# Kernel optimization log

Measured on AMD Instinct MI355X. Metric: run time of the kernel, lower is better.

The kernel has to match this reference:

```python
import jax, jax.numpy as jnp
import numpy as np

N, K, D, E, H, A = 50000, 12, 64, 64, 4, 16
C = 2 * D + E  # concat feature len = 192
EPS = 1e-5


def masked_bn(x, mask, gamma, beta, axes):
    # BatchNorm (training-mode batch stats) computed only over valid (mask==1) entries,
    # matching torch BN applied to PackedSequence.data.
    cnt = jnp.sum(mask) * 1.0
    mean = jnp.sum(x * mask, axis=axes) / cnt
    var = jnp.sum(jnp.square(x - mean) * mask, axis=axes) / cnt
    return gamma * (x - mean) / jnp.sqrt(var + EPS) + beta


def setup_inputs() -> dict:
    key = jax.random.key(0)
    ks = jax.random.split(key, 16)
    node_features = jax.random.normal(ks[0], (N, D), jnp.float32)
    edge_features = jax.random.normal(ks[1], (N, K, E), jnp.float32)
    neighbor_indices = jax.random.randint(ks[2], (N, K), 0, N, jnp.int32)
    # contiguous-prefix masks (pack_padded_sequence semantics), lengths in [1, K]
    lens = jax.random.randint(ks[3], (N,), 1, K + 1)
    neighbor_masks = (jnp.arange(K)[None, :] < lens[:, None]).astype(jnp.float32)
    s = 0.05
    W_edge = jax.random.normal(ks[4], (C, E), jnp.float32) * s
    b_edge = jnp.zeros((E,), jnp.float32)
    g_edge_bn = jnp.ones((E,), jnp.float32)
    b_edge_bn = jnp.zeros((E,), jnp.float32)
    W_att1 = jax.random.normal(ks[5], (H, C, A), jnp.float32) * s
    b_att1 = jnp.zeros((H, A), jnp.float32)
    W_att2 = jax.random.normal(ks[6], (H, A), jnp.float32) * s
    b_att2 = jnp.zeros((H,), jnp.float32)
    W_val = jax.random.normal(ks[7], (H, C, A), jnp.float32) * s
    b_val = jnp.zeros((H, A), jnp.float32)
    g_att_bn = jnp.ones((H, A), jnp.float32)
    b_att_bn = jnp.zeros((H, A), jnp.float32)
    g_out_bn = jnp.ones((D,), jnp.float32)
    b_out_bn = jnp.zeros((D,), jnp.float32)
    return dict(node_features=node_features, edge_features=edge_features,
                neighbor_indices=neighbor_indices, neighbor_masks=neighbor_masks,
                W_edge=W_edge, b_edge=b_edge, g_edge_bn=g_edge_bn, b_edge_bn=b_edge_bn,
                W_att1=W_att1, b_att1=b_att1, W_att2=W_att2, b_att2=b_att2,
                W_val=W_val, b_val=b_val, g_att_bn=g_att_bn, b_att_bn=b_att_bn,
                g_out_bn=g_out_bn, b_out_bn=b_out_bn)


def reference(node_features, edge_features, neighbor_indices, neighbor_masks,
              W_edge, b_edge, g_edge_bn, b_edge_bn,
              W_att1, b_att1, W_att2, b_att2, W_val, b_val,
              g_att_bn, b_att_bn, g_out_bn, b_out_bn):
    sp = jax.nn.softplus
    # fix rows with zero neighbors: mask -> [1, 0, ..., 0]
    lens = neighbor_masks.sum(axis=1)
    fix_row = jnp.zeros((K,), neighbor_masks.dtype).at[0].set(1.0)
    mask = jnp.where((lens == 0)[:, None], fix_row[None, :], neighbor_masks)  # [N,K]
    m3 = mask[:, :, None]            # [N,K,1]
    m4 = mask[:, :, None, None]      # [N,K,1,1]

    nbr = node_features[neighbor_indices]                         # [N,K,D] gather
    self_f = jnp.broadcast_to(node_features[:, None, :], (N, K, D))
    pair = jnp.concatenate([self_f, nbr], axis=2)                 # [N,K,2D]

    c1 = jnp.concatenate([pair, edge_features], axis=2)           # [N,K,C]
    e_lin = c1 @ W_edge + b_edge                                  # [N,K,E]
    e_bn = masked_bn(e_lin, m3, g_edge_bn, b_edge_bn, axes=(0, 1))
    # padded entries contribute 0 from the packed BN output (pad_packed zero-fills)
    edge_updated = sp(edge_features + e_bn * m3)                  # [N,K,E]

    c2 = jnp.concatenate([pair, edge_updated], axis=2)            # [N,K,C]

    # attention MLP per head: Linear(C->A) + softplus + Linear(A->1)
    h1 = sp(jnp.einsum('nkc,hca->nkha', c2, W_att1) + b_att1)     # [N,K,H,A]
    logits = jnp.einsum('nkha,ha->nkh', h1, W_att2) + b_att2      # [N,K,H]
    logits = jnp.where(mask[:, :, None] > 0, logits, -jnp.inf)
    att = jax.nn.softmax(logits, axis=1)                          # [N,K,H]

    v = jnp.einsum('nkc,hca->nkha', c2, W_val) + b_val            # [N,K,H,A]
    p = att[:, :, :, None] * v                                    # [N,K,H,A]
    p_bn = masked_bn(p, m4, g_att_bn, b_att_bn, axes=(0, 1))
    head_feats = sp(p_bn) * m4                                    # zero at pads
    pooled = jnp.sum(head_feats, axis=1).reshape(N, H * A)        # [N,D]

    # output BN over nodes (H*A == D, so no after-concat linear)
    mean = pooled.mean(axis=0)
    var = jnp.mean(jnp.square(pooled - mean), axis=0)
    out = g_out_bn * (pooled - mean) / jnp.sqrt(var + EPS) + b_out_bn

    node_updated = node_features + out                            # residual
    return node_updated, edge_updated
```

## Files before the change

### kernel.cpp

```cpp
#include <hip/hip_runtime.h>
#include <math.h>

#define NN 50000
#define KK 12

typedef unsigned short u16;
typedef __attribute__((ext_vector_type(4))) float f32x4;
typedef __attribute__((ext_vector_type(8))) short short8;

__device__ inline u16 f2b(float x){
  union { float f; unsigned u; } v; v.f = x;
  unsigned r = v.u + 0x7fffu + ((v.u >> 16) & 1u);
  return (u16)(r >> 16);
}
__device__ inline float b2f(u16 b){
  union { unsigned u; float f; } v; v.u = ((unsigned)b) << 16; return v.f;
}
__device__ inline float sp_(float x){
  return fmaxf(x, 0.f) + __logf(1.f + __expf(-fabsf(x)));
}
__device__ inline f32x4 mfma16(short8 a, short8 b, f32x4 c){
  return __builtin_amdgcn_mfma_f32_16x16x32_bf16(a, b, c, 0, 0, 0);
}
__device__ inline short8 ldfrag(const u16* lds, int base, int lane, int ks){
  return *(const short8*)&lds[(base + (lane & 15))*72 + ks*32 + (lane >> 4)*8];
}
__device__ inline short8 ldwfrag(const u16* wmat, int lane, int nt, int ks){
  return *(const short8*)&wmat[(nt*16 + (lane & 15))*64 + ks*32 + (lane >> 4)*8];
}
__device__ inline void stage_tile192(const float* src, u16* ldsA, int t){
  #pragma unroll
  for (int i = 0; i < 12; ++i){
    int f4 = t + i*256;
    int m = f4 >> 4, d = (f4 & 15) * 4;
    const float4 v = *(const float4*)(src + m*64 + d);
    ushort4 b; b.x = f2b(v.x); b.y = f2b(v.y); b.z = f2b(v.z); b.w = f2b(v.w);
    *(ushort4*)&ldsA[m*72 + d] = b;
  }
}

__global__ void kw_conv(const float* We, const float* Wa, const float* Wv, u16* wb){
  int gid = blockIdx.x*256 + threadIdx.x;
  if (gid >= 9*4096) return;
  int mat = gid >> 12, rem = gid & 4095;
  int j = rem >> 6, d = rem & 63;
  int fam = mat / 3, part = mat % 3;
  int c = part*64 + d;
  float v;
  if (fam == 0) v = We[c*64 + j];
  else {
    const float* W = (fam == 1) ? Wa : Wv;
    v = W[(j >> 4)*3072 + c*16 + (j & 15)];
  }
  wb[mat*4096 + j*64 + d] = f2b(v);
}

__global__ void km_mask(const float* masks, float* maskf, float* stats){
  int t = threadIdx.x;
  int n = blockIdx.x*256 + t;
  float len = 0.f;
  if (n < NN){
    float row[KK];
    #pragma unroll
    for (int k = 0; k < KK; ++k){ row[k] = masks[n*KK + k]; len += row[k]; }
    if (len == 0.f){
      #pragma unroll
      for (int k = 0; k < KK; ++k) row[k] = (k == 0) ? 1.f : 0.f;
      len = 1.f;
    }
    #pragma unroll
    for (int k = 0; k < KK; ++k) maskf[n*KK + k] = row[k];
  }
  __shared__ float red[256];
  red[t] = len; __syncthreads();
  for (int s = 128; s > 0; s >>= 1){ if (t < s) red[t] += red[t + s]; __syncthreads(); }
  if (t == 0) atomicAdd(&stats[0], red[0]);
}

__global__ __launch_bounds__(256,4) void kp_proj(const float* node, const u16* wb,
    float* ps_e, float* ps_a, float* ps_v, u16* pn_e, u16* pn_a, u16* pn_v){
  __shared__ u16 ldsA[64*72];
  int t = threadIdx.x;
  int node0 = blockIdx.x*64;
  #pragma unroll
  for (int i = 0; i < 4; ++i){
    int f4 = t + i*256;
    int m = f4 >> 4, d = (f4 & 15)*4;
    float4 v = make_float4(0.f,0.f,0.f,0.f);
    if (node0 + m < NN) v = *(const float4*)(node + (size_t)(node0 + m)*64 + d);
    ushort4 b; b.x=f2b(v.x); b.y=f2b(v.y); b.z=f2b(v.z); b.w=f2b(v.w);
    *(ushort4*)&ldsA[m*72 + d] = b;
  }
  __syncthreads();
  int lane = t & 63, w = t >> 6;
  int m0 = w*16;
  short8 a0 = ldfrag(ldsA, m0, lane, 0);
  short8 a1 = ldfrag(ldsA, m0, lane, 1);
  float* psArr[3] = {ps_e, ps_a, ps_v};
  u16*  pnArr[3] = {pn_e, pn_a, pn_v};
  #pragma unroll
  for (int p = 0; p < 6; ++p){
    const u16* W = wb + ((p % 3)*3 + (p / 3))*4096;
    #pragma unroll
    for (int nt = 0; nt < 4; ++nt){
      short8 b0 = ldwfrag(W, lane, nt, 0);
      short8 b1 = ldwfrag(W, lane, nt, 1);
      f32x4 acc = {0.f,0.f,0.f,0.f};
      acc = mfma16(a0, b0, acc);
      acc = mfma16(a1, b1, acc);
      int col = nt*16 + (lane & 15);
      #pragma unroll
      for (int r = 0; r < 4; ++r){
        int nrow = node0 + m0 + (lane >> 4)*4 + r;
        if (nrow < NN){
          if (p < 3) psArr[p][(size_t)nrow*64 + col] = acc[r];
          else       pnArr[p-3][(size_t)nrow*64 + col] = f2b(acc[r]);
        }
      }
    }
  }
}

__global__ __launch_bounds__(256,4) void k1_estats(const float* edgef, const int* nidx,
    const float* maskf, const float* ps_e, const u16* pn_e, const float* b_edge,
    const u16* wb, float* stats){
  __shared__ u16 ldsA[192*72];
  __shared__ int rPs[192]; __shared__ int rPn[192]; __shared__ float rM[192];
  __shared__ float sred[128];
  int t = threadIdx.x;
  int node0 = blockIdx.x*16;
  int e0 = node0*KK;
  stage_tile192(edgef + (size_t)e0*64, ldsA, t);
  if (t < 192){ rPs[t] = (node0 + t/KK)*64; rPn[t] = nidx[e0 + t]*64; rM[t] = maskf[e0 + t]; }
  if (t < 128) sred[t] = 0.f;
  __syncthreads();
  int lane = t & 63, w = t >> 6;
  const u16* We_ = wb + 2*4096;
  float be4[4];
  #pragma unroll
  for (int nt = 0; nt < 4; ++nt) be4[nt] = b_edge[nt*16 + (lane & 15)];
  #pragma unroll
  for (int mi = 0; mi < 3; ++mi){
    int mt = w + mi*4;
    short8 a0 = ldfrag(ldsA, mt*16, lane, 0);
    short8 a1 = ldfrag(ldsA, mt*16, lane, 1);
    #pragma unroll
    for (int nt = 0; nt < 4; ++nt){
      short8 b0 = ldwfrag(We_, lane, nt, 0);
      short8 b1 = ldwfrag(We_, lane, nt, 1);
      f32x4 acc = {0.f,0.f,0.f,0.f};
      acc = mfma16(a0, b0, acc);
      acc = mfma16(a1, b1, acc);
      int col = nt*16 + (lane & 15);
      float s = 0.f, q = 0.f;
      #pragma unroll
      for (int r = 0; r < 4; ++r){
        int row = mt*16 + (lane >> 4)*4 + r;
        float v = acc[r] + ps_e[rPs[row] + col] + b2f(pn_e[rPn[row] + col]) + be4[nt];
        float m = rM[row];
        s += v*m; q += v*v*m;
      }
      s += __shfl_xor(s, 16); s += __shfl_xor(s, 32);
      q += __shfl_xor(q, 16); q += __shfl_xor(q, 32);
      if (lane < 16){ atomicAdd(&sred[col], s); atomicAdd(&sred[64 + col], q); }
    }
  }
  __syncthreads();
  if (t < 128) atomicAdd(&stats[64 + t], sred[t]);
}

__global__ void k_fin(const float* g, const float* b, float* stats, int sumoff, int outoff, float cntfix){
  int j = threadIdx.x;
  float cnt = (cntfix > 0.f) ? cntfix : stats[0];
  float mean = stats[sumoff + j] / cnt;
  float var = stats[sumoff + 64 + j] / cnt - mean*mean;
  var = fmaxf(var, 0.f);
  float A = g[j] / sqrtf(var + 1e-5f);
  stats[outoff + j] = A;
  stats[outoff + 64 + j] = b[j] - mean*A;
}

__global__ __launch_bounds__(256,4) void k3_main(const float* edgef, const int* nidx,
    const float* maskf, const float* ps_e, const u16* pn_e, const float* ps_a, const u16* pn_a,
    const float* ps_v, const u16* pn_v, const float* b_edge, const float* b_att1,
    const float* W_att2, const float* b_att2, const float* b_val,
    const u16* wb, float* stats, float* out_edge, float* att_out, u16* p_out){
  __shared__ u16 ldsA[192*72];
  __shared__ float ldsLA[192*4];
  __shared__ int rPs[192]; __shared__ int rPn[192]; __shared__ float rM[192];
  __shared__ float sred[128];
  int t = threadIdx.x;
  int node0 = blockIdx.x*16;
  int e0 = node0*KK;
  stage_tile192(edgef + (size_t)e0*64, ldsA, t);
  if (t < 192){ rPs[t] = (node0 + t/KK)*64; rPn[t] = nidx[e0 + t]*64; rM[t] = maskf[e0 + t]; }
  if (t < 128) sred[t] = 0.f;
  __syncthreads();
  int lane = t & 63, w = t >> 6;
  int cl = lane & 15;

  {
    const u16* W = wb + 2*4096;
    float Ae4[4], Be4[4], be4[4];
    #pragma unroll
    for (int nt = 0; nt < 4; ++nt){
      int col = nt*16 + cl;
      Ae4[nt] = stats[192 + col]; Be4[nt] = stats[256 + col]; be4[nt] = b_edge[col];
    }
    #pragma unroll
    for (int mi = 0; mi < 3; ++mi){
      int mt = w + mi*4;
      short8 a0 = ldfrag(ldsA, mt*16, lane, 0);
      short8 a1 = ldfrag(ldsA, mt*16, lane, 1);
      #pragma unroll
      for (int nt = 0; nt < 4; ++nt){
        short8 b0 = ldwfrag(W, lane, nt, 0);
        short8 b1 = ldwfrag(W, lane, nt, 1);
        f32x4 acc = {0.f,0.f,0.f,0.f};
        acc = mfma16(a0, b0, acc);
        acc = mfma16(a1, b1, acc);
        int col = nt*16 + cl;
        #pragma unroll
        for (int r = 0; r < 4; ++r){
          int row = mt*16 + (lane >> 4)*4 + r;
          float elin = acc[r] + ps_e[rPs[row] + col] + b2f(pn_e[rPn[row] + col]) + be4[nt];
          float ebn = Ae4[nt]*elin + Be4[nt];
          float orig = b2f(ldsA[row*72 + col]);
          float eu = sp_(orig + ebn*rM[row]);
          out_edge[((size_t)e0 + row)*64 + col] = eu;
          ldsA[row*72 + col] = f2b(eu);
        }
      }
    }
  }
  __syncthreads();
  {
    const u16* W = wb + 5*4096;
    float w24[4], ba4[4];
    #pragma unroll
    for (int nt = 0; nt < 4; ++nt){
      int col = nt*16 + cl;
      w24[nt] = W_att2[col]; ba4[nt] = b_att1[col];
    }
    #pragma unroll
    for (int mi = 0; mi < 3; ++mi){
      int mt = w + mi*4;
      short8 a0 = ldfrag(ldsA, mt*16, lane, 0);
      short8 a1 = ldfrag(ldsA, mt*16, lane, 1);
      #pragma unroll
      for (int nt = 0; nt < 4; ++nt){
        short8 b0 = ldwfrag(W, lane, nt, 0);
        short8 b1 = ldwfrag(W, lane, nt, 1);
        f32x4 acc = {0.f,0.f,0.f,0.f};
        acc = mfma16(a0, b0, acc);
        acc = mfma16(a1, b1, acc);
        int col = nt*16 + cl;
        #pragma unroll
        for (int r = 0; r < 4; ++r){
          int row = mt*16 + (lane >> 4)*4 + r;
          float h1 = sp_(acc[r] + ps_a[rPs[row] + col] + b2f(pn_a[rPn[row] + col]) + ba4[nt]);
          float lg = h1 * w24[nt];
          lg += __shfl_xor(lg, 1); lg += __shfl_xor(lg, 2);
          lg += __shfl_xor(lg, 4); lg += __shfl_xor(lg, 8);
          if (cl == 0) ldsLA[row*4 + nt] = lg + b_att2[nt];
        }
      }
    }
  }
  __syncthreads();
  if (t < 64){
    int nl = t >> 2, h = t & 3;
    float lrow[KK], mrow[KK];
    #pragma unroll
    for (int k = 0; k < KK; ++k){ lrow[k] = ldsLA[(nl*KK + k)*4 + h]; mrow[k] = rM[nl*KK + k]; }
    float mx = -3.0e38f;
    #pragma unroll
    for (int k = 0; k < KK; ++k) if (mrow[k] > 0.f) mx = fmaxf(mx, lrow[k]);
    float ssum = 0.f; float ee[KK];
    #pragma unroll
    for (int k = 0; k < KK; ++k){ float e = (mrow[k] > 0.f) ? __expf(lrow[k] - mx) : 0.f; ee[k] = e; ssum += e; }
    float inv = 1.f / ssum;
    #pragma unroll
    for (int k = 0; k < KK; ++k){
      float a = ee[k]*inv;
      ldsLA[(nl*KK + k)*4 + h] = a;
      att_out[((size_t)(node0 + nl)*KK + k)*4 + h] = a;
    }
  }
  __syncthreads();
  {
    const u16* W = wb + 8*4096;
    float bv4[4];
    #pragma unroll
    for (int nt = 0; nt < 4; ++nt) bv4[nt] = b_val[nt*16 + cl];
    #pragma unroll
    for (int mi = 0; mi < 3; ++mi){
      int mt = w + mi*4;
      short8 a0 = ldfrag(ldsA, mt*16, lane, 0);
      short8 a1 = ldfrag(ldsA, mt*16, lane, 1);
      #pragma unroll
      for (int nt = 0; nt < 4; ++nt){
        short8 b0 = ldwfrag(W, lane, nt, 0);
        short8 b1 = ldwfrag(W, lane, nt, 1);
        f32x4 acc = {0.f,0.f,0.f,0.f};
        acc = mfma16(a0, b0, acc);
        acc = mfma16(a1, b1, acc);
        int col = nt*16 + cl;
        float s = 0.f, q = 0.f;
        #pragma unroll
        for (int r = 0; r < 4; ++r){
          int row = mt*16 + (lane >> 4)*4 + r;
          float v = acc[r] + ps_v[rPs[row] + col] + b2f(pn_v[rPn[row] + col]) + bv4[nt];
          float p = ldsLA[row*4 + nt] * v;
          float m = rM[row];
          s += p*m; q += p*p*m;
          if (p_out) p_out[((size_t)e0 + row)*64 + col] = f2b(p);
        }
        s += __shfl_xor(s, 16); s += __shfl_xor(s, 32);
        q += __shfl_xor(q, 16); q += __shfl_xor(q, 32);
        if (lane < 16){ atomicAdd(&sred[col], s); atomicAdd(&sred[64 + col], q); }
      }
    }
  }
  __syncthreads();
  if (t < 128) atomicAdd(&stats[320 + t], sred[t]);
}

__global__ void k5_stream(const u16* pbuf, const float* maskf, float* stats, float* pooled){
  __shared__ float sred[128];
  int t = threadIdx.x;
  int node0 = blockIdx.x*16;
  int col = t & 63;
  if (t < 128) sred[t] = 0.f;
  __syncthreads();
  float Ap = stats[448 + col], Bp = stats[512 + col];
  float s = 0.f, q = 0.f;
  #pragma unroll
  for (int i = 0; i < 4; ++i){
    int n = node0 + (t >> 6) + i*4;
    float acc = 0.f;
    #pragma unroll
    for (int k = 0; k < KK; ++k){
      float m = maskf[n*KK + k];
      float p = b2f(pbuf[((size_t)(n*KK + k))*64 + col]);
      acc += sp_(Ap*p + Bp) * m;
    }
    pooled[(size_t)n*64 + col] = acc;
    s += acc; q += acc*acc;
  }
  atomicAdd(&sred[col], s); atomicAdd(&sred[64 + col], q);
  __syncthreads();
  if (t < 128) atomicAdd(&stats[576 + t], sred[t]);
}

__global__ __launch_bounds__(256,4) void k5_rec(const float* eu, const int* nidx,
    const float* maskf, const float* ps_v, const u16* pn_v, const float* b_val,
    const u16* wb, const float* att_in, float* stats, float* pooled){
  __shared__ u16 ldsA[192*72];
  __shared__ float ldsAtt[192*4];
  __shared__ float pool[16*64];
  __shared__ int rPs[192]; __shared__ int rPn[192]; __shared__ float rM[192];
  __shared__ float sred[128];
  int t = threadIdx.x;
  int node0 = blockIdx.x*16;
  int e0 = node0*KK;
  stage_tile192(eu + (size_t)e0*64, ldsA, t);
  if (t < 192){ rPs[t] = (node0 + t/KK)*64; rPn[t] = nidx[e0 + t]*64; rM[t] = maskf[e0 + t]; }
  #pragma unroll
  for (int i = 0; i < 3; ++i){ int q = t + i*256; ldsAtt[q] = att_in[(size_t)e0*4 + q]; }
  #pragma unroll
  for (int i = 0; i < 4; ++i) pool[t + i*256] = 0.f;
  if (t < 128) sred[t] = 0.f;
  __syncthreads();
  int lane = t & 63, w = t >> 6;
  int cl = lane & 15;
  const u16* W = wb + 8*4096;
  float bv4[4], Ap4[4], Bp4[4];
  #pragma unroll
  for (int nt = 0; nt < 4; ++nt){
    int col = nt*16 + cl;
    bv4[nt] = b_val[col]; Ap4[nt] = stats[448 + col]; Bp4[nt] = stats[512 + col];
  }
  #pragma unroll
  for (int mi = 0; mi < 3; ++mi){
    int mt = w + mi*4;
    short8 a0 = ldfrag(ldsA, mt*16, lane, 0);
    short8 a1 = ldfrag(ldsA, mt*16, lane, 1);
    #pragma unroll
    for (int nt = 0; nt < 4; ++nt){
      short8 b0 = ldwfrag(W, lane, nt, 0);
      short8 b1 = ldwfrag(W, lane, nt, 1);
      f32x4 acc = {0.f,0.f,0.f,0.f};
      acc = mfma16(a0, b0, acc);
      acc = mfma16(a1, b1, acc);
      int col = nt*16 + cl;
      #pragma unroll
      for (int r = 0; r < 4; ++r){
        int row = mt*16 + (lane >> 4)*4 + r;
        float v = acc[r] + ps_v[rPs[row] + col] + b2f(pn_v[rPn[row] + col]) + bv4[nt];
        float p = ldsAtt[row*4 + nt] * v;
        float head = sp_(Ap4[nt]*p + Bp4[nt]) * rM[row];
        atomicAdd(&pool[(row/KK)*64 + col], head);
      }
    }
  }
  __syncthreads();
  int ch = t & 63;
  float s = 0.f, q = 0.f;
  #pragma unroll
  for (int i = 0; i < 4; ++i){
    int qi = t + i*256;
    float val = pool[qi];
    pooled[((size_t)(node0 + (qi >> 6)))*64 + ch] = val;
    s += val; q += val*val;
  }
  atomicAdd(&sred[ch], s); atomicAdd(&sred[64 + ch], q);
  __syncthreads();
  if (t < 128) atomicAdd(&stats[576 + t], sred[t]);
}

__global__ void k7_out(const float* node, const float* stats, float* out){
  int i = blockIdx.x*256 + threadIdx.x;
  if (i < NN*64){
    int ch = i & 63;
    float pooled = out[i];
    out[i] = node[i] + stats[704 + ch]*pooled + stats[768 + ch];
  }
}

extern "C" void kernel_launch(void* const* d_in, const int* in_sizes, int n_in,
                              void* d_out, int out_size, void* d_ws, size_t ws_size,
                              hipStream_t stream){
  const float* node   = (const float*)d_in[0];
  const float* edgef  = (const float*)d_in[1];
  const int*   nidx   = (const int*)d_in[2];
  const float* masks  = (const float*)d_in[3];
  const float* We     = (const float*)d_in[4];
  const float* b_edge = (const float*)d_in[5];
  const float* g_ebn  = (const float*)d_in[6];
  const float* b_ebn  = (const float*)d_in[7];
  const float* Wa1    = (const float*)d_in[8];
  const float* b_att1 = (const float*)d_in[9];
  const float* Wa2    = (const float*)d_in[10];
  const float* b_att2 = (const float*)d_in[11];
  const float* Wv     = (const float*)d_in[12];
  const float* b_val  = (const float*)d_in[13];
  const float* g_abn  = (const float*)d_in[14];
  const float* b_abn  = (const float*)d_in[15];
  const float* g_obn  = (const float*)d_in[16];
  const float* b_obn  = (const float*)d_in[17];

  float* ps_e   = (float*)d_ws;
  float* ps_a   = ps_e   + (size_t)NN*64;
  float* ps_v   = ps_a   + (size_t)NN*64;
  float* maskf  = ps_v   + (size_t)NN*64;
  float* att    = maskf  + (size_t)NN*KK;
  float* stats  = att    + (size_t)NN*KK*4;
  u16*   pn_e   = (u16*)(stats + 1024);
  u16*   pn_a   = pn_e   + (size_t)NN*64;
  u16*   pn_v   = pn_a   + (size_t)NN*64;
  u16*   wb     = pn_v   + (size_t)NN*64;
  u16*   pbuf   = wb     + 9*4096;
  size_t need   = (size_t)((char*)(pbuf + (size_t)NN*KK*64) - (char*)d_ws);
  bool   use_p  = (ws_size >= need);

  float* out_node = (float*)d_out;
  float* out_edge = out_node + (size_t)NN*64;

  hipMemsetAsync(stats, 0, 1024*sizeof(float), stream);
  kw_conv<<<144, 256, 0, stream>>>(We, Wa1, Wv, wb);
  km_mask<<<(NN + 255)/256, 256, 0, stream>>>(masks, maskf, stats);
  kp_proj<<<(NN + 63)/64, 256, 0, stream>>>(node, wb, ps_e, ps_a, ps_v, pn_e, pn_a, pn_v);
  k1_estats<<<NN/16, 256, 0, stream>>>(edgef, nidx, maskf, ps_e, pn_e, b_edge, wb, stats);
  k_fin<<<1, 64, 0, stream>>>(g_ebn, b_ebn, stats, 64, 192, 0.f);
  k3_main<<<NN/16, 256, 0, stream>>>(edgef, nidx, maskf, ps_e, pn_e, ps_a, pn_a, ps_v, pn_v,
      b_edge, b_att1, Wa2, b_att2, b_val, wb, stats, out_edge, att, use_p ? pbuf : (u16*)nullptr);
  k_fin<<<1, 64, 0, stream>>>(g_abn, b_abn, stats, 320, 448, 0.f);
  if (use_p)
    k5_stream<<<NN/16, 256, 0, stream>>>(pbuf, maskf, stats, out_node);
  else
    k5_rec<<<NN/16, 256, 0, stream>>>(out_edge, nidx, maskf, ps_v, pn_v, b_val, wb, att, stats, out_node);
  k_fin<<<1, 64, 0, stream>>>(g_obn, b_obn, stats, 576, 704, (float)NN);
  k7_out<<<(NN*64 + 255)/256, 256, 0, stream>>>(node, stats, out_node);
}
```

Baseline: 826.9 us.

## Fuse attention and value GEMMs in k3, shrink LDS metadata, vectorize k5_stream

In k3_main the attention-logit and value projections now run in a single pass over the A fragments. The value results are kept in registers as packed bf16 until the softmax finishes, which removes one reload of the LDS tiles and one phase of weight fragment reads. Per-row LDS arrays are slimmed by computing the self-node row with a multiply-shift instead of storing rPs, and by storing the mask as a byte; launch bounds rise to 5 blocks per SM. The attention output write is skipped when the streaming path is used. k5_stream now processes 4 channels per thread with vector loads and stores. The trade-off is higher register pressure from holding the value results, and a small precision loss from rounding v to bf16 before the multiply by attention.

```diff
diff --git a/kernel.cpp b/kernel.cpp
--- a/kernel.cpp
+++ b/kernel.cpp
@@ -5,6 +5,7 @@
 #define KK 12
 
 typedef unsigned short u16;
+typedef unsigned char u8;
 typedef __attribute__((ext_vector_type(4))) float f32x4;
 typedef __attribute__((ext_vector_type(8))) short short8;
 
@@ -22,6 +23,7 @@
 __device__ inline f32x4 mfma16(short8 a, short8 b, f32x4 c){
   return __builtin_amdgcn_mfma_f32_16x16x32_bf16(a, b, c, 0, 0, 0);
 }
+__device__ inline int nl_(int row){ return (row*171) >> 11; }
 __device__ inline short8 ldfrag(const u16* lds, int base, int lane, int ks){
   return *(const short8*)&lds[(base + (lane & 15))*72 + ks*32 + (lane >> 4)*8];
 }
@@ -121,24 +123,26 @@
   }
 }
 
-__global__ __launch_bounds__(256,4) void k1_estats(const float* edgef, const int* nidx,
+__global__ __launch_bounds__(256,5) void k1_estats(const float* edgef, const int* nidx,
     const float* maskf, const float* ps_e, const u16* pn_e, const float* b_edge,
     const u16* wb, float* stats){
   __shared__ u16 ldsA[192*72];
-  __shared__ int rPs[192]; __shared__ int rPn[192]; __shared__ float rM[192];
+  __shared__ int rPn[192]; __shared__ u8 m8[192];
   __shared__ float sred[128];
   int t = threadIdx.x;
   int node0 = blockIdx.x*16;
   int e0 = node0*KK;
+  int psb = node0*64;
   stage_tile192(edgef + (size_t)e0*64, ldsA, t);
-  if (t < 192){ rPs[t] = (node0 + t/KK)*64; rPn[t] = nidx[e0 + t]*64; rM[t] = maskf[e0 + t]; }
+  if (t < 192){ rPn[t] = nidx[e0 + t]*64; m8[t] = (u8)maskf[e0 + t]; }
   if (t < 128) sred[t] = 0.f;
   __syncthreads();
   int lane = t & 63, w = t >> 6;
+  int cl = lane & 15;
   const u16* We_ = wb + 2*4096;
   float be4[4];
   #pragma unroll
-  for (int nt = 0; nt < 4; ++nt) be4[nt] = b_edge[nt*16 + (lane & 15)];
+  for (int nt = 0; nt < 4; ++nt) be4[nt] = b_edge[nt*16 + cl];
   #pragma unroll
   for (int mi = 0; mi < 3; ++mi){
     int mt = w + mi*4;
@@ -151,13 +155,13 @@
       f32x4 acc = {0.f,0.f,0.f,0.f};
       acc = mfma16(a0, b0, acc);
       acc = mfma16(a1, b1, acc);
-      int col = nt*16 + (lane & 15);
+      int col = nt*16 + cl;
       float s = 0.f, q = 0.f;
       #pragma unroll
       for (int r = 0; r < 4; ++r){
         int row = mt*16 + (lane >> 4)*4 + r;
-        float v = acc[r] + ps_e[rPs[row] + col] + b2f(pn_e[rPn[row] + col]) + be4[nt];
-        float m = rM[row];
+        float v = acc[r] + ps_e[psb + nl_(row)*64 + col] + b2f(pn_e[rPn[row] + col]) + be4[nt];
+        float m = (float)m8[row];
         s += v*m; q += v*v*m;
       }
       s += __shfl_xor(s, 16); s += __shfl_xor(s, 32);
@@ -180,20 +184,21 @@
   stats[outoff + 64 + j] = b[j] - mean*A;
 }
 
-__global__ __launch_bounds__(256,4) void k3_main(const float* edgef, const int* nidx,
+__global__ __launch_bounds__(256,5) void k3_main(const float* edgef, const int* nidx,
     const float* maskf, const float* ps_e, const u16* pn_e, const float* ps_a, const u16* pn_a,
     const float* ps_v, const u16* pn_v, const float* b_edge, const float* b_att1,
     const float* W_att2, const float* b_att2, const float* b_val,
     const u16* wb, float* stats, float* out_edge, float* att_out, u16* p_out){
   __shared__ u16 ldsA[192*72];
   __shared__ float ldsLA[192*4];
-  __shared__ int rPs[192]; __shared__ int rPn[192]; __shared__ float rM[192];
+  __shared__ int rPn[192]; __shared__ u8 m8[192];
   __shared__ float sred[128];
   int t = threadIdx.x;
   int node0 = blockIdx.x*16;
   int e0 = node0*KK;
+  int psb = node0*64;
   stage_tile192(edgef + (size_t)e0*64, ldsA, t);
-  if (t < 192){ rPs[t] = (node0 + t/KK)*64; rPn[t] = nidx[e0 + t]*64; rM[t] = maskf[e0 + t]; }
+  if (t < 192){ rPn[t] = nidx[e0 + t]*64; m8[t] = (u8)maskf[e0 + t]; }
   if (t < 128) sred[t] = 0.f;
   __syncthreads();
   int lane = t & 63, w = t >> 6;
@@ -223,10 +228,10 @@
         #pragma unroll
         for (int r = 0; r < 4; ++r){
           int row = mt*16 + (lane >> 4)*4 + r;
-          float elin = acc[r] + ps_e[rPs[row] + col] + b2f(pn_e[rPn[row] + col]) + be4[nt];
+          float elin = acc[r] + ps_e[psb + nl_(row)*64 + col] + b2f(pn_e[rPn[row] + col]) + be4[nt];
           float ebn = Ae4[nt]*elin + Be4[nt];
           float orig = b2f(ldsA[row*72 + col]);
-          float eu = sp_(orig + ebn*rM[row]);
+          float eu = sp_(orig + ebn*(float)m8[row]);
           out_edge[((size_t)e0 + row)*64 + col] = eu;
           ldsA[row*72 + col] = f2b(eu);
         }
@@ -234,13 +239,15 @@
     }
   }
   __syncthreads();
+  unsigned vpk[3][4][2];
   {
-    const u16* W = wb + 5*4096;
-    float w24[4], ba4[4];
+    const u16* Wa = wb + 5*4096;
+    const u16* Wv = wb + 8*4096;
+    float w24[4], ba4[4], bv4[4];
     #pragma unroll
     for (int nt = 0; nt < 4; ++nt){
       int col = nt*16 + cl;
-      w24[nt] = W_att2[col]; ba4[nt] = b_att1[col];
+      w24[nt] = W_att2[col]; ba4[nt] = b_att1[col]; bv4[nt] = b_val[col];
     }
     #pragma unroll
     for (int mi = 0; mi < 3; ++mi){
@@ -249,8 +256,8 @@
       short8 a1 = ldfrag(ldsA, mt*16, lane, 1);
       #pragma unroll
       for (int nt = 0; nt < 4; ++nt){
-        short8 b0 = ldwfrag(W, lane, nt, 0);
-        short8 b1 = ldwfrag(W, lane, nt, 1);
+        short8 b0 = ldwfrag(Wa, lane, nt, 0);
+        short8 b1 = ldwfrag(Wa, lane, nt, 1);
         f32x4 acc = {0.f,0.f,0.f,0.f};
         acc = mfma16(a0, b0, acc);
         acc = mfma16(a1, b1, acc);
@@ -258,97 +265,113 @@
         #pragma unroll
         for (int r = 0; r < 4; ++r){
           int row = mt*16 + (lane >> 4)*4 + r;
-          float h1 = sp_(acc[r] + ps_a[rPs[row] + col] + b2f(pn_a[rPn[row] + col]) + ba4[nt]);
+          float h1 = sp_(acc[r] + ps_a[psb + nl_(row)*64 + col] + b2f(pn_a[rPn[row] + col]) + ba4[nt]);
           float lg = h1 * w24[nt];
           lg += __shfl_xor(lg, 1); lg += __shfl_xor(lg, 2);
           lg += __shfl_xor(lg, 4); lg += __shfl_xor(lg, 8);
           if (cl == 0) ldsLA[row*4 + nt] = lg + b_att2[nt];
         }
       }
-    }
-  }
-  __syncthreads();
-  if (t < 64){
-    int nl = t >> 2, h = t & 3;
-    float lrow[KK], mrow[KK];
-    #pragma unroll
-    for (int k = 0; k < KK; ++k){ lrow[k] = ldsLA[(nl*KK + k)*4 + h]; mrow[k] = rM[nl*KK + k]; }
-    float mx = -3.0e38f;
-    #pragma unroll
-    for (int k = 0; k < KK; ++k) if (mrow[k] > 0.f) mx = fmaxf(mx, lrow[k]);
-    float ssum = 0.f; float ee[KK];
-    #pragma unroll
-    for (int k = 0; k < KK; ++k){ float e = (mrow[k] > 0.f) ? __expf(lrow[k] - mx) : 0.f; ee[k] = e; ssum += e; }
-    float inv = 1.f / ssum;
-    #pragma unroll
-    for (int k = 0; k < KK; ++k){
-      float a = ee[k]*inv;
-      ldsLA[(nl*KK + k)*4 + h] = a;
-      att_out[((size_t)(node0 + nl)*KK + k)*4 + h] = a;
-    }
-  }
-  __syncthreads();
-  {
-    const u16* W = wb + 8*4096;
-    float bv4[4];
-    #pragma unroll
-    for (int nt = 0; nt < 4; ++nt) bv4[nt] = b_val[nt*16 + cl];
-    #pragma unroll
-    for (int mi = 0; mi < 3; ++mi){
-      int mt = w + mi*4;
-      short8 a0 = ldfrag(ldsA, mt*16, lane, 0);
-      short8 a1 = ldfrag(ldsA, mt*16, lane, 1);
       #pragma unroll
       for (int nt = 0; nt < 4; ++nt){
-        short8 b0 = ldwfrag(W, lane, nt, 0);
-        short8 b1 = ldwfrag(W, lane, nt, 1);
+        short8 b0 = ldwfrag(Wv, lane, nt, 0);
+        short8 b1 = ldwfrag(Wv, lane, nt, 1);
         f32x4 acc = {0.f,0.f,0.f,0.f};
         acc = mfma16(a0, b0, acc);
         acc = mfma16(a1, b1, acc);
         int col = nt*16 + cl;
-        float s = 0.f, q = 0.f;
         #pragma unroll
         for (int r = 0; r < 4; ++r){
           int row = mt*16 + (lane >> 4)*4 + r;
-          float v = acc[r] + ps_v[rPs[row] + col] + b2f(pn_v[rPn[row] + col]) + bv4[nt];
+          float v = acc[r] + ps_v[psb + nl_(row)*64 + col] + b2f(pn_v[rPn[row] + col]) + bv4[nt];
+          unsigned vb = (unsigned)f2b(v);
+          if ((r & 1) == 0) vpk[mi][nt][r >> 1] = vb;
+          else              vpk[mi][nt][r >> 1] |= (vb << 16);
+        }
+      }
+    }
+  }
+  __syncthreads();
+  if (t < 64){
+    int nl = t >> 2, h = t & 3;
+    float lrow[KK], mrow[KK];
+    #pragma unroll
+    for (int k = 0; k < KK; ++k){ lrow[k] = ldsLA[(nl*KK + k)*4 + h]; mrow[k] = (float)m8[nl*KK + k]; }
+    float mx = -3.0e38f;
+    #pragma unroll
+    for (int k = 0; k < KK; ++k) if (mrow[k] > 0.f) mx = fmaxf(mx, lrow[k]);
+    float ssum = 0.f; float ee[KK];
+    #pragma unroll
+    for (int k = 0; k < KK; ++k){ float e = (mrow[k] > 0.f) ? __expf(lrow[k] - mx) : 0.f; ee[k] = e; ssum += e; }
+    float inv = 1.f / ssum;
+    #pragma unroll
+    for (int k = 0; k < KK; ++k){
+      float a = ee[k]*inv;
+      ldsLA[(nl*KK + k)*4 + h] = a;
+      if (att_out) att_out[((size_t)(node0 + nl)*KK + k)*4 + h] = a;
+    }
+  }
+  __syncthreads();
+  {
+    float s[4] = {0.f,0.f,0.f,0.f}, q[4] = {0.f,0.f,0.f,0.f};
+    #pragma unroll
+    for (int mi = 0; mi < 3; ++mi){
+      int mt = w + mi*4;
+      #pragma unroll
+      for (int nt = 0; nt < 4; ++nt){
+        int col = nt*16 + cl;
+        #pragma unroll
+        for (int r = 0; r < 4; ++r){
+          int row = mt*16 + (lane >> 4)*4 + r;
+          unsigned pk = vpk[mi][nt][r >> 1];
+          float v = b2f((u16)((r & 1) ? (pk >> 16) : (pk & 0xffff)));
           float p = ldsLA[row*4 + nt] * v;
-          float m = rM[row];
-          s += p*m; q += p*p*m;
+          float m = (float)m8[row];
+          s[nt] += p*m; q[nt] += p*p*m;
           if (p_out) p_out[((size_t)e0 + row)*64 + col] = f2b(p);
         }
-        s += __shfl_xor(s, 16); s += __shfl_xor(s, 32);
-        q += __shfl_xor(q, 16); q += __shfl_xor(q, 32);
-        if (lane < 16){ atomicAdd(&sred[col], s); atomicAdd(&sred[64 + col], q); }
-      }
+      }
+    }
+    #pragma unroll
+    for (int nt = 0; nt < 4; ++nt){
+      float ss = s[nt], qq = q[nt];
+      ss += __shfl_xor(ss, 16); ss += __shfl_xor(ss, 32);
+      qq += __shfl_xor(qq, 16); qq += __shfl_xor(qq, 32);
+      if (lane < 16){ atomicAdd(&sred[nt*16 + cl], ss); atomicAdd(&sred[64 + nt*16 + cl], qq); }
     }
   }
   __syncthreads();
   if (t < 128) atomicAdd(&stats[320 + t], sred[t]);
 }
 
-__global__ void k5_stream(const u16* pbuf, const float* maskf, float* stats, float* pooled){
+__global__ __launch_bounds__(256,8) void k5_stream(const u16* pbuf, const float* maskf,
+    float* stats, float* pooled){
   __shared__ float sred[128];
   int t = threadIdx.x;
   int node0 = blockIdx.x*16;
-  int col = t & 63;
+  int n = node0 + (t >> 4);
+  int cg = (t & 15)*4;
   if (t < 128) sred[t] = 0.f;
   __syncthreads();
-  float Ap = stats[448 + col], Bp = stats[512 + col];
-  float s = 0.f, q = 0.f;
-  #pragma unroll
-  for (int i = 0; i < 4; ++i){
-    int n = node0 + (t >> 6) + i*4;
-    float acc = 0.f;
-    #pragma unroll
-    for (int k = 0; k < KK; ++k){
-      float m = maskf[n*KK + k];
-      float p = b2f(pbuf[((size_t)(n*KK + k))*64 + col]);
-      acc += sp_(Ap*p + Bp) * m;
-    }
-    pooled[(size_t)n*64 + col] = acc;
-    s += acc; q += acc*acc;
-  }
-  atomicAdd(&sred[col], s); atomicAdd(&sred[64 + col], q);
+  float Ap[4], Bp[4];
+  #pragma unroll
+  for (int j = 0; j < 4; ++j){ Ap[j] = stats[448 + cg + j]; Bp[j] = stats[512 + cg + j]; }
+  float acc[4] = {0.f,0.f,0.f,0.f};
+  #pragma unroll
+  for (int k = 0; k < KK; ++k){
+    float m = maskf[n*KK + k];
+    ushort4 pv = *(const ushort4*)&pbuf[((size_t)(n*KK + k))*64 + cg];
+    acc[0] += sp_(Ap[0]*b2f(pv.x) + Bp[0]) * m;
+    acc[1] += sp_(Ap[1]*b2f(pv.y) + Bp[1]) * m;
+    acc[2] += sp_(Ap[2]*b2f(pv.z) + Bp[2]) * m;
+    acc[3] += sp_(Ap[3]*b2f(pv.w) + Bp[3]) * m;
+  }
+  *(float4*)&pooled[(size_t)n*64 + cg] = make_float4(acc[0], acc[1], acc[2], acc[3]);
+  #pragma unroll
+  for (int j = 0; j < 4; ++j){
+    atomicAdd(&sred[cg + j], acc[j]);
+    atomicAdd(&sred[64 + cg + j], acc[j]*acc[j]);
+  }
   __syncthreads();
   if (t < 128) atomicAdd(&stats[576 + t], sred[t]);
 }
@@ -359,13 +382,14 @@
   __shared__ u16 ldsA[192*72];
   __shared__ float ldsAtt[192*4];
   __shared__ float pool[16*64];
-  __shared__ int rPs[192]; __shared__ int rPn[192]; __shared__ float rM[192];
+  __shared__ int rPn[192]; __shared__ u8 m8[192];
   __shared__ float sred[128];
   int t = threadIdx.x;
   int node0 = blockIdx.x*16;
   int e0 = node0*KK;
+  int psb = node0*64;
   stage_tile192(eu + (size_t)e0*64, ldsA, t);
-  if (t < 192){ rPs[t] = (node0 + t/KK)*64; rPn[t] = nidx[e0 + t]*64; rM[t] = maskf[e0 + t]; }
+  if (t < 192){ rPn[t] = nidx[e0 + t]*64; m8[t] = (u8)maskf[e0 + t]; }
   #pragma unroll
   for (int i = 0; i < 3; ++i){ int q = t + i*256; ldsAtt[q] = att_in[(size_t)e0*4 + q]; }
   #pragma unroll
@@ -397,10 +421,10 @@
       #pragma unroll
       for (int r = 0; r < 4; ++r){
         int row = mt*16 + (lane >> 4)*4 + r;
-        float v = acc[r] + ps_v[rPs[row] + col] + b2f(pn_v[rPn[row] + col]) + bv4[nt];
+        float v = acc[r] + ps_v[psb + nl_(row)*64 + col] + b2f(pn_v[rPn[row] + col]) + bv4[nt];
         float p = ldsAtt[row*4 + nt] * v;
-        float head = sp_(Ap4[nt]*p + Bp4[nt]) * rM[row];
-        atomicAdd(&pool[(row/KK)*64 + col], head);
+        float head = sp_(Ap4[nt]*p + Bp4[nt]) * (float)m8[row];
+        atomicAdd(&pool[nl_(row)*64 + col], head);
       }
     }
   }
@@ -474,7 +498,8 @@
   k1_estats<<<NN/16, 256, 0, stream>>>(edgef, nidx, maskf, ps_e, pn_e, b_edge, wb, stats);
   k_fin<<<1, 64, 0, stream>>>(g_ebn, b_ebn, stats, 64, 192, 0.f);
   k3_main<<<NN/16, 256, 0, stream>>>(edgef, nidx, maskf, ps_e, pn_e, ps_a, pn_a, ps_v, pn_v,
-      b_edge, b_att1, Wa2, b_att2, b_val, wb, stats, out_edge, att, use_p ? pbuf : (u16*)nullptr);
+      b_edge, b_att1, Wa2, b_att2, b_val, wb, stats, out_edge,
+      use_p ? (float*)nullptr : att, use_p ? pbuf : (u16*)nullptr);
   k_fin<<<1, 64, 0, stream>>>(g_abn, b_abn, stats, 320, 448, 0.f);
   if (use_p)
     k5_stream<<<NN/16, 256, 0, stream>>>(pbuf, maskf, stats, out_node);
```

Measured after the change: 1.383 ms. +67.2%, slower.
